# Kernel optimization log

Hardware: AMD Instinct MI355X
Metric: run time of the kernel (lower is better)

## Reference

```python
import jax, jax.numpy as jnp
import numpy as np

B, L, D = 4, 16384, 128          # batch, voxels per sample, d_model
DI, DS, DTR, K = 256, 16, 8, 4   # d_inner, d_state, dt_rank, conv kernel
N = B * L
EPS = 1e-5


def setup_inputs() -> dict:
    key = jax.random.key(0)
    ks = jax.random.split(key, 12)
    s = 0.02
    feats = jax.random.normal(ks[0], (N, D), jnp.float32)
    coords_xyz = jax.random.randint(ks[1], (N, 3), 0, 1024, jnp.int32)
    # per-batch Morton permutation + its inverse
    perm = jnp.stack([jax.random.permutation(jax.random.fold_in(ks[2], i), L) for i in range(B)]).astype(jnp.int32)
    inv_perm = jnp.argsort(perm, axis=1).astype(jnp.int32)
    return {
        'feats': feats,
        'pos_w': jax.random.normal(ks[3], (3, D), jnp.float32) * s,
        'pos_b': jnp.zeros((D,), jnp.float32),
        'rms_w': jnp.ones((D,), jnp.float32),
        'in_proj_w': jax.random.normal(ks[4], (D, 2 * DI), jnp.float32) * s,
        'conv_w': jax.random.normal(ks[5], (DI, K), jnp.float32) * s,
        'conv_b': jnp.zeros((DI,), jnp.float32),
        'x_proj_w': jax.random.normal(ks[6], (DI, DTR + 2 * DS), jnp.float32) * s,
        'dt_proj_w': jax.random.normal(ks[7], (DTR, DI), jnp.float32) * s,
        'dt_proj_b': jax.random.normal(ks[8], (DI,), jnp.float32) * 0.1,
        'A_log': jnp.log(jnp.broadcast_to(jnp.arange(1.0, DS + 1.0, dtype=jnp.float32), (DI, DS))),
        'D_param': jnp.ones((DI,), jnp.float32),
        'out_proj_w': jax.random.normal(ks[9], (DI, D), jnp.float32) * s,
        'ln_w': jnp.ones((D,), jnp.float32),
        'ln_b': jnp.zeros((D,), jnp.float32),
        'coords_xyz': coords_xyz,
        'perm': perm,
        'inv_perm': inv_perm,
    }


def _gssm(feats, pos_w, pos_b, rms_w, in_proj_w, conv_w, conv_b, x_proj_w,
          dt_proj_w, dt_proj_b, A_log, D_param, out_proj_w, ln_w, ln_b,
          coords_xyz, perm, inv_perm):
    # positional embedding of voxel coords
    pe = coords_xyz.astype(jnp.float32) @ pos_w + pos_b            # [N, D]
    h = (feats + pe).reshape(B, L, D)
    # gather into Morton order (per-batch fancy index)
    hm = jnp.take_along_axis(h, perm[:, :, None].astype(jnp.int32), axis=1)  # [B, L, D]
    # Mamba block: RMSNorm then mixer (block returns mixer output only)
    x = hm * jax.lax.rsqrt(jnp.mean(hm * hm, axis=-1, keepdims=True) + EPS) * rms_w
    xz = x @ in_proj_w                                             # [B, L, 2*DI]
    xi, z = xz[..., :DI], xz[..., DI:]
    # depthwise causal conv1d, kernel K
    xp = jnp.pad(xi, ((0, 0), (K - 1, 0), (0, 0)))
    xc = conv_b + sum(xp[:, j:j + L, :] * conv_w[:, j] for j in range(K))
    xc = jax.nn.silu(xc)                                           # [B, L, DI]
    dbc = xc @ x_proj_w                                            # [B, L, DTR+2*DS]
    dt, Bm, Cm = dbc[..., :DTR], dbc[..., DTR:DTR + DS], dbc[..., DTR + DS:]
    dt = jax.nn.softplus(dt @ dt_proj_w + dt_proj_b)               # [B, L, DI]
    A = -jnp.exp(A_log)                                            # [DI, DS]

    def step(hst, inp):
        x_t, dt_t, b_t, c_t = inp                                  # [B,DI],[B,DI],[B,DS],[B,DS]
        hst = jnp.exp(dt_t[..., None] * A) * hst + (dt_t * x_t)[..., None] * b_t[:, None, :]
        return hst, jnp.einsum('bds,bs->bd', hst, c_t)

    h0 = jnp.zeros((B, DI, DS), xc.dtype)
    _, ys = jax.lax.scan(step, h0, (xc.transpose(1, 0, 2), dt.transpose(1, 0, 2),
                                    Bm.transpose(1, 0, 2), Cm.transpose(1, 0, 2)))
    y = ys.transpose(1, 0, 2) + xc * D_param                       # [B, L, DI]
    y = y * jax.nn.silu(z)
    out = y @ out_proj_w                                           # [B, L, D]
    # scatter back to original voxel order
    out = jnp.take_along_axis(out, inv_perm[:, :, None].astype(jnp.int32), axis=1).reshape(N, D)
    # post-SSM LayerNorm
    mu = jnp.mean(out, axis=-1, keepdims=True)
    var = jnp.mean((out - mu) ** 2, axis=-1, keepdims=True)
    return (out - mu) * jax.lax.rsqrt(var + EPS) * ln_w + ln_b


def reference(feats, pos_w, pos_b, rms_w, in_proj_w, conv_w, conv_b, x_proj_w,
              dt_proj_w, dt_proj_b, A_log, D_param, out_proj_w, ln_w, ln_b,
              coords_xyz, perm, inv_perm):
    return _gssm(feats, pos_w, pos_b, rms_w, in_proj_w, conv_w, conv_b, x_proj_w,
                 dt_proj_w, dt_proj_b, A_log, D_param, out_proj_w, ln_w, ln_b,
                 coords_xyz, perm, inv_perm)
```

## Files before the change

kernel.cpp:

```cpp
#include <hip/hip_runtime.h>
#include <hip/hip_bf16.h>
#include <math.h>

#define B_   4
#define L_   16384
#define D_   128
#define DI_  256
#define DS_  16
#define DTR_ 8
#define N_   65536
#define NC_  128
#define LC_  128
#define TW_  16
#define TP_  260
#define EPS_ 1e-5f

typedef __hip_bfloat16 bf16;
typedef __attribute__((ext_vector_type(8))) short short8;
typedef __attribute__((ext_vector_type(4))) float f32x4;

__device__ __forceinline__ bool probe_bf16(const void* Dp) {
  return ((const unsigned*)Dp)[0] == 0x3F803F80u;
}
__device__ __forceinline__ float ldin(const void* p, size_t i, bool isb) {
  return isb ? __bfloat162float(((const bf16*)p)[i]) : ((const float*)p)[i];
}
__device__ __forceinline__ float4 ld4(const void* p, size_t i4, bool isb) {
  if (!isb) return ((const float4*)p)[i4];
  const ushort4 v = ((const ushort4*)p)[i4];
  float4 r;
  r.x = __uint_as_float((unsigned)v.x << 16);
  r.y = __uint_as_float((unsigned)v.y << 16);
  r.z = __uint_as_float((unsigned)v.z << 16);
  r.w = __uint_as_float((unsigned)v.w << 16);
  return r;
}
__device__ __forceinline__ void splitbf(float v, ushort& hi, ushort& lo) {
  bf16 h = __float2bfloat16(v);
  float rem = v - __bfloat162float(h);
  bf16 l = __float2bfloat16(rem);
  hi = *(ushort*)&h;
  lo = *(ushort*)&l;
}


__global__ __launch_bounds__(256) void k_xnorm(
    const void* __restrict__ feats, const void* __restrict__ pos_w,
    const void* __restrict__ pos_b, const void* __restrict__ rms_w,
    const int* __restrict__ coords, const int* __restrict__ perm,
    const void* __restrict__ Dprobe,
    ushort* __restrict__ xh, ushort* __restrict__ xl) {
  const bool isb = probe_bf16(Dprobe);
  int wv = threadIdx.x >> 6, lane = threadIdx.x & 63;
  int p = blockIdx.x * 4 + wv;
  int b = p >> 14;
  int srow = b * L_ + perm[p];
  float cx = (float)coords[srow*3+0];
  float cy = (float)coords[srow*3+1];
  float cz = (float)coords[srow*3+2];
  int i0 = lane, i1 = lane + 64;
  float h0 = ldin(feats,(size_t)srow*D_ + i0,isb) + cx*ldin(pos_w,i0,isb) + cy*ldin(pos_w,D_+i0,isb)
           + cz*ldin(pos_w,2*D_+i0,isb) + ldin(pos_b,i0,isb);
  float h1 = ldin(feats,(size_t)srow*D_ + i1,isb) + cx*ldin(pos_w,i1,isb) + cy*ldin(pos_w,D_+i1,isb)
           + cz*ldin(pos_w,2*D_+i1,isb) + ldin(pos_b,i1,isb);
  float ss = h0*h0 + h1*h1;
  #pragma unroll
  for (int off = 32; off; off >>= 1) ss += __shfl_xor(ss, off);
  float r = 1.0f / sqrtf(ss * (1.f/128.f) + EPS_);
  float v0 = h0 * r * ldin(rms_w,i0,isb);
  float v1 = h1 * r * ldin(rms_w,i1,isb);
  ushort a, bq;
  splitbf(v0, a, bq);
  xh[(size_t)p*D_ + i0] = a; xl[(size_t)p*D_ + i0] = bq;
  splitbf(v1, a, bq);
  xh[(size_t)p*D_ + i1] = a; xl[(size_t)p*D_ + i1] = bq;
}

__global__ __launch_bounds__(256) void k_prepw(
    const void* __restrict__ Win, const void* __restrict__ Dprobe,
    ushort* __restrict__ wth, ushort* __restrict__ wtl) {
  const bool isb = probe_bf16(Dprobe);
  int idx = blockIdx.x * 256 + threadIdx.x;
  int k = idx >> 9, n = idx & 511;
  float v = ldin(Win, (size_t)k*512 + n, isb);
  ushort a, b;
  splitbf(v, a, b);
  wth[(size_t)n*128 + k] = a;
  wtl[(size_t)n*128 + k] = b;
}

__global__ __launch_bounds__(256) void k_inproj(
    const ushort* __restrict__ xh, const ushort* __restrict__ xl,
    const ushort* __restrict__ wth, const ushort* __restrict__ wtl,
    float* __restrict__ xiT, float* __restrict__ zB) {
  __shared__ short Ah[64*136];
  __shared__ short Al[64*136];
  __shared__ short Bh[32*136];
  __shared__ short Bl[32*136];
  int tid = threadIdx.x;
  int T0 = blockIdx.x * 64;
  int lane = tid & 63, w = tid >> 6;
  {
    int k0 = (tid & 15) * 8;
    int m0 = tid >> 4;
    #pragma unroll
    for (int mi = 0; mi < 4; ++mi) {
      int m = m0 + 16*mi;
      *(short8*)&Ah[m*136 + k0] = *(const short8*)&xh[(size_t)(T0+m)*128 + k0];
      *(short8*)&Al[m*136 + k0] = *(const short8*)&xl[(size_t)(T0+m)*128 + k0];
    }
  }
  __syncthreads();
  int mloc = lane & 15, quad = lane >> 4;
  short8 afh[4], afl[4];
  #pragma unroll
  for (int ks = 0; ks < 4; ++ks) {
    int ka = ks*32 + quad*8;
    afh[ks] = *(const short8*)&Ah[(w*16 + mloc)*136 + ka];
    afl[ks] = *(const short8*)&Al[(w*16 + mloc)*136 + ka];
  }
  for (int ct = 0; ct < 16; ++ct) {
    int C0 = ct * 32;
    __syncthreads();
    {
      int k0 = (tid & 15) * 8;
      int n0 = tid >> 4;
      #pragma unroll
      for (int ni = 0; ni < 2; ++ni) {
        int n = n0 + 16*ni;
        *(short8*)&Bh[n*136 + k0] = *(const short8*)&wth[(size_t)(C0+n)*128 + k0];
        *(short8*)&Bl[n*136 + k0] = *(const short8*)&wtl[(size_t)(C0+n)*128 + k0];
      }
    }
    __syncthreads();
    #pragma unroll
    for (int nt = 0; nt < 2; ++nt) {
      f32x4 acc = {0.f, 0.f, 0.f, 0.f};
      #pragma unroll
      for (int ks = 0; ks < 4; ++ks) {
        int kb = ks*32 + quad*8;
        short8 bh = *(const short8*)&Bh[(nt*16 + mloc)*136 + kb];
        short8 bl = *(const short8*)&Bl[(nt*16 + mloc)*136 + kb];
        acc = __builtin_amdgcn_mfma_f32_16x16x32_bf16(afh[ks], bh, acc, 0, 0, 0);
        acc = __builtin_amdgcn_mfma_f32_16x16x32_bf16(afl[ks], bh, acc, 0, 0, 0);
        acc = __builtin_amdgcn_mfma_f32_16x16x32_bf16(afh[ks], bl, acc, 0, 0, 0);
      }
      int col = C0 + nt*16 + mloc;
      int trow = T0 + w*16 + quad*4;
      if (col < 256) {
        *(float4*)&xiT[(size_t)col*N_ + trow] = make_float4(acc[0], acc[1], acc[2], acc[3]);
      } else {
        int zc = col - 256;
        #pragma unroll
        for (int r = 0; r < 4; ++r)
          zB[(size_t)(trow + r)*256 + zc] = acc[r];
      }
    }
  }
}

__global__ __launch_bounds__(256) void k_conv_s(
    const float* __restrict__ xiT, const void* __restrict__ conv_w,
    const void* __restrict__ conv_b, const void* __restrict__ Dprobe,
    float* __restrict__ xcT) {
  const bool isb = probe_bf16(Dprobe);
  int idx = blockIdx.x * 256 + threadIdx.x;
  int c = idx >> 16;
  int t = idx & 65535;
  int l = t & (L_-1);
  const float* row = xiT + (size_t)c * N_;
  float acc = ldin(conv_b, c, isb);
  if (l >= 3) acc += row[t-3] * ldin(conv_w, c*4+0, isb);
  if (l >= 2) acc += row[t-2] * ldin(conv_w, c*4+1, isb);
  if (l >= 1) acc += row[t-1] * ldin(conv_w, c*4+2, isb);
  acc += row[t] * ldin(conv_w, c*4+3, isb);
  xcT[(size_t)c*N_ + t] = acc / (1.f + __expf(-acc));
}

__global__ __launch_bounds__(256) void k_xproj(
    const float* __restrict__ xcT, const void* __restrict__ xW,
    const void* __restrict__ dtW, const void* __restrict__ dtb,
    const void* __restrict__ Dprobe,
    float* __restrict__ dtT, float* __restrict__ BmB, float* __restrict__ CmB) {
  const bool isb = probe_bf16(Dprobe);
  __shared__ float lds[15488];
  int tid = threadIdx.x;
  int T0 = blockIdx.x * 128;
  int t = tid & 127, half = tid >> 7;
  #pragma unroll
  for (int p = 0; p < 10; ++p) {
    int idx = p*256 + tid;
    *(float4*)&lds[idx*4] = ld4(xW, idx, isb);
  }
  __syncthreads();
  float acc[40];
  #pragma unroll
  for (int q = 0; q < 40; ++q) acc[q] = 0.f;
  for (int c = 0; c < 128; c += 2) {
    int ch0 = half*128 + c, ch1 = ch0 + 1;
    float v0 = xcT[(size_t)ch0*N_ + T0 + t];
    float v1 = xcT[(size_t)ch1*N_ + T0 + t];
    const float* w0 = &lds[ch0*40];
    const float* w1 = &lds[ch1*40];
    #pragma unroll
    for (int q = 0; q < 10; ++q) {
      float4 a = *(const float4*)&w0[q*4];
      float4 b = *(const float4*)&w1[q*4];
      acc[q*4+0] += v0*a.x + v1*b.x;
      acc[q*4+1] += v0*a.y + v1*b.y;
      acc[q*4+2] += v0*a.z + v1*b.z;
      acc[q*4+3] += v0*a.w + v1*b.w;
    }
  }
  if (half == 1) {
    #pragma unroll
    for (int q = 0; q < 40; ++q) lds[10240 + t*41 + q] = acc[q];
  }
  __syncthreads();
  if (half == 0) {
    #pragma unroll
    for (int q = 0; q < 40; ++q) acc[q] += lds[10240 + t*41 + q];
  }
  __syncthreads();
  if (half == 0) {
    *(float4*)&BmB[(size_t)(T0+t)*16 + 0]  = make_float4(acc[8],  acc[9],  acc[10], acc[11]);
    *(float4*)&BmB[(size_t)(T0+t)*16 + 4]  = make_float4(acc[12], acc[13], acc[14], acc[15]);
    *(float4*)&BmB[(size_t)(T0+t)*16 + 8]  = make_float4(acc[16], acc[17], acc[18], acc[19]);
    *(float4*)&BmB[(size_t)(T0+t)*16 + 12] = make_float4(acc[20], acc[21], acc[22], acc[23]);
    *(float4*)&CmB[(size_t)(T0+t)*16 + 0]  = make_float4(acc[24], acc[25], acc[26], acc[27]);
    *(float4*)&CmB[(size_t)(T0+t)*16 + 4]  = make_float4(acc[28], acc[29], acc[30], acc[31]);
    *(float4*)&CmB[(size_t)(T0+t)*16 + 8]  = make_float4(acc[32], acc[33], acc[34], acc[35]);
    *(float4*)&CmB[(size_t)(T0+t)*16 + 12] = make_float4(acc[36], acc[37], acc[38], acc[39]);
    #pragma unroll
    for (int r = 0; r < 8; ++r) lds[10240 + t*9 + r] = acc[r];
  }
  #pragma unroll
  for (int p = 0; p < 8; ++p) lds[11392 + p*256 + tid] = ldin(dtW, p*256 + tid, isb);
  lds[13440 + tid] = ldin(dtb, tid, isb);
  __syncthreads();
  int t2 = tid & 127, dhalf = tid >> 7;
  float db[8];
  #pragma unroll
  for (int r = 0; r < 8; ++r) db[r] = lds[10240 + t2*9 + r];
  for (int dd = 0; dd < 128; ++dd) {
    int d = dhalf*128 + dd;
    float pre = lds[13440 + d];
    #pragma unroll
    for (int r = 0; r < 8; ++r) pre += db[r] * lds[11392 + r*256 + d];
    float sp = (pre > 20.f) ? pre : log1pf(__expf(pre));
    dtT[(size_t)d*N_ + T0 + t2] = sp;
  }
}

__global__ __launch_bounds__(256) void k_scan1(
    const float* __restrict__ dtT, const float* __restrict__ xcT,
    const float* __restrict__ BmB, const void* __restrict__ A_log,
    const void* __restrict__ Dprobe, float* __restrict__ Pb, float* __restrict__ Sb) {
  const bool isb = probe_bf16(Dprobe);
  __shared__ float sdt[TW_*TP_];
  __shared__ float sxc[TW_*TP_];
  __shared__ float sbm[LC_*16];
  int tid = threadIdx.x;
  int blk = blockIdx.x;
  int b = blk >> 7, ch = blk & 127;
  int T0 = b * L_ + ch * LC_;
  int d = tid;
  #pragma unroll
  for (int p = 0; p < 2; ++p) {
    int f = (p*256 + tid) * 4;
    *(float4*)&sbm[f] = *(const float4*)&BmB[(size_t)T0*16 + f];
  }
  float Al[16];
  #pragma unroll
  for (int s = 0; s < 16; ++s) Al[s] = -__expf(ldin(A_log, d*16 + s, isb));
  float h[16];
  #pragma unroll
  for (int s = 0; s < 16; ++s) h[s] = 0.f;
  float sumdt = 0.f;
  for (int it = 0; it < LC_; it += TW_) {
    __syncthreads();
    #pragma unroll
    for (int p = 0; p < 4; ++p) {
      int idx = p*256 + tid;
      int d2 = idx >> 2;
      int i4 = (idx & 3) * 4;
      float4 v = *(const float4*)&dtT[(size_t)d2*N_ + T0 + it + i4];
      float4 w = *(const float4*)&xcT[(size_t)d2*N_ + T0 + it + i4];
      sdt[(i4+0)*TP_ + d2] = v.x; sdt[(i4+1)*TP_ + d2] = v.y;
      sdt[(i4+2)*TP_ + d2] = v.z; sdt[(i4+3)*TP_ + d2] = v.w;
      sxc[(i4+0)*TP_ + d2] = w.x; sxc[(i4+1)*TP_ + d2] = w.y;
      sxc[(i4+2)*TP_ + d2] = w.z; sxc[(i4+3)*TP_ + d2] = w.w;
    }
    __syncthreads();
    #pragma unroll
    for (int i = 0; i < TW_; ++i) {
      float dtv = sdt[i*TP_ + d];
      float xcv = sxc[i*TP_ + d];
      sumdt += dtv;
      float du = dtv * xcv;
      const float* bmr = &sbm[(it+i)*16];
      #pragma unroll
      for (int s = 0; s < 16; ++s)
        h[s] = __expf(dtv * Al[s]) * h[s] + du * bmr[s];
    }
  }
  size_t rec = ((size_t)blk*256 + d) * 16;
  #pragma unroll
  for (int s = 0; s < 16; ++s) {
    Sb[rec + s] = h[s];
    Pb[rec + s] = __expf(Al[s] * sumdt);
  }
}

__global__ __launch_bounds__(256) void k_scan2(
    const float* __restrict__ Pb, const float* __restrict__ Sb, float* __restrict__ Hin) {
  int tid = blockIdx.x * 256 + threadIdx.x;
  int b = tid >> 12, r = tid & 4095;
  float h = 0.f;
  for (int ch = 0; ch < NC_; ++ch) {
    size_t rec = ((size_t)(b*NC_ + ch)) * 4096 + r;
    Hin[rec] = h;
    h = Pb[rec] * h + Sb[rec];
  }
}

__global__ __launch_bounds__(256) void k_scan3(
    const float* __restrict__ dtT, const float* __restrict__ xcT,
    const float* __restrict__ BmB, const float* __restrict__ CmB,
    const void* __restrict__ A_log, const void* __restrict__ Dp,
    const float* __restrict__ Hin, float* __restrict__ zyg) {
  const bool isb = probe_bf16(Dp);
  __shared__ float sdt[TW_*TP_];
  __shared__ float sxc[TW_*TP_];
  __shared__ float sbm[LC_*16];
  __shared__ float scm[LC_*16];
  int tid = threadIdx.x;
  int blk = blockIdx.x;
  int b = blk >> 7, ch = blk & 127;
  int T0 = b * L_ + ch * LC_;
  int d = tid;
  #pragma unroll
  for (int p = 0; p < 2; ++p) {
    int f = (p*256 + tid) * 4;
    *(float4*)&sbm[f] = *(const float4*)&BmB[(size_t)T0*16 + f];
    *(float4*)&scm[f] = *(const float4*)&CmB[(size_t)T0*16 + f];
  }
  float Al[16];
  #pragma unroll
  for (int s = 0; s < 16; ++s) Al[s] = -__expf(ldin(A_log, d*16 + s, isb));
  float h[16];
  size_t rec = ((size_t)blk*256 + d) * 16;
  #pragma unroll
  for (int s = 0; s < 16; ++s) h[s] = Hin[rec + s];
  float Dv = ldin(Dp, d, isb);
  for (int it = 0; it < LC_; it += TW_) {
    __syncthreads();
    #pragma unroll
    for (int p = 0; p < 4; ++p) {
      int idx = p*256 + tid;
      int d2 = idx >> 2;
      int i4 = (idx & 3) * 4;
      float4 v = *(const float4*)&dtT[(size_t)d2*N_ + T0 + it + i4];
      float4 w = *(const float4*)&xcT[(size_t)d2*N_ + T0 + it + i4];
      sdt[(i4+0)*TP_ + d2] = v.x; sdt[(i4+1)*TP_ + d2] = v.y;
      sdt[(i4+2)*TP_ + d2] = v.z; sdt[(i4+3)*TP_ + d2] = v.w;
      sxc[(i4+0)*TP_ + d2] = w.x; sxc[(i4+1)*TP_ + d2] = w.y;
      sxc[(i4+2)*TP_ + d2] = w.z; sxc[(i4+3)*TP_ + d2] = w.w;
    }
    __syncthreads();
    #pragma unroll
    for (int i = 0; i < TW_; ++i) {
      float dtv = sdt[i*TP_ + d];
      float xcv = sxc[i*TP_ + d];
      float du = dtv * xcv;
      const float* bmr = &sbm[(it+i)*16];
      const float* cmr = &scm[(it+i)*16];
      float y = 0.f;
      #pragma unroll
      for (int s = 0; s < 16; ++s) {
        h[s] = __expf(dtv * Al[s]) * h[s] + du * bmr[s];
        y += h[s] * cmr[s];
      }
      float yv = y + xcv * Dv;
      size_t zi = (size_t)(T0 + it + i)*256 + d;
      float zv = zyg[zi];
      float sil = zv / (1.f + __expf(-zv));
      zyg[zi] = yv * sil;
    }
  }
}

__global__ __launch_bounds__(256) void k_outproj(
    const float* __restrict__ yg, const void* __restrict__ W2,
    const void* __restrict__ Dprobe, float* __restrict__ outp) {
  const bool isb = probe_bf16(Dprobe);
  __shared__ float As[64*68];
  __shared__ float Bs[64*128];
  int tid = threadIdx.x;
  int T0 = blockIdx.x * 64;
  int tm = tid & 15, tn = tid >> 4;
  float acc[4][8] = {{0.f}};
  for (int kb = 0; kb < 256; kb += 64) {
    {
      int m = tid & 63, kq = tid >> 6;
      #pragma unroll
      for (int r = 0; r < 4; ++r) {
        int k0 = kq*16 + r*4;
        float4 v = *(const float4*)&yg[(size_t)(T0+m)*256 + kb + k0];
        As[(k0+0)*68+m] = v.x; As[(k0+1)*68+m] = v.y;
        As[(k0+2)*68+m] = v.z; As[(k0+3)*68+m] = v.w;
      }
      int n = (tid & 31)*4, kq2 = tid >> 5;
      #pragma unroll
      for (int p = 0; p < 8; ++p) {
        int k = kq2 + p*8;
        float4 w = ld4(W2, ((size_t)(kb+k)*128 + n) >> 2, isb);
        *(float4*)&Bs[k*128 + n] = w;
      }
    }
    __syncthreads();
    #pragma unroll 4
    for (int k = 0; k < 64; ++k) {
      float4 a  = *(const float4*)&As[k*68 + tm*4];
      float4 b0 = *(const float4*)&Bs[k*128 + tn*8];
      float4 b1 = *(const float4*)&Bs[k*128 + tn*8 + 4];
      float am[4] = {a.x, a.y, a.z, a.w};
      float bn[8] = {b0.x, b0.y, b0.z, b0.w, b1.x, b1.y, b1.z, b1.w};
      #pragma unroll
      for (int mi = 0; mi < 4; ++mi)
        #pragma unroll
        for (int ni = 0; ni < 8; ++ni)
          acc[mi][ni] += am[mi] * bn[ni];
    }
    __syncthreads();
  }
  #pragma unroll
  for (int mi = 0; mi < 4; ++mi) {
    size_t m = (size_t)(T0 + tm*4 + mi);
    *(float4*)&outp[m*128 + tn*8]     = make_float4(acc[mi][0], acc[mi][1], acc[mi][2], acc[mi][3]);
    *(float4*)&outp[m*128 + tn*8 + 4] = make_float4(acc[mi][4], acc[mi][5], acc[mi][6], acc[mi][7]);
  }
}

__global__ __launch_bounds__(256) void k_ln(
    const float* __restrict__ outp, const int* __restrict__ perm,
    const void* __restrict__ ln_w, const void* __restrict__ ln_b,
    const void* __restrict__ Dprobe, void* __restrict__ out) {
  const bool isb = probe_bf16(Dprobe);
  int wv = threadIdx.x >> 6, lane = threadIdx.x & 63;
  int p = blockIdx.x * 4 + wv;
  int b = p >> 14;
  int dest = b * L_ + perm[p];
  float v0 = outp[(size_t)p*128 + lane];
  float v1 = outp[(size_t)p*128 + lane + 64];
  float s1 = v0 + v1, s2 = v0*v0 + v1*v1;
  #pragma unroll
  for (int off = 32; off; off >>= 1) {
    s1 += __shfl_xor(s1, off);
    s2 += __shfl_xor(s2, off);
  }
  float mean = s1 * (1.f/128.f);
  float var  = s2 * (1.f/128.f) - mean*mean;
  float r = 1.0f / sqrtf(var + EPS_);
  float o0 = (v0 - mean)*r*ldin(ln_w,lane,isb)    + ldin(ln_b,lane,isb);
  float o1 = (v1 - mean)*r*ldin(ln_w,lane+64,isb) + ldin(ln_b,lane+64,isb);
  if (isb) {
    ((bf16*)out)[(size_t)dest*128 + lane]      = __float2bfloat16(o0);
    ((bf16*)out)[(size_t)dest*128 + lane + 64] = __float2bfloat16(o1);
  } else {
    ((float*)out)[(size_t)dest*128 + lane]      = o0;
    ((float*)out)[(size_t)dest*128 + lane + 64] = o1;
  }
}

extern "C" void kernel_launch(void* const* d_in, const int* in_sizes, int n_in,
                              void* d_out, int out_size, void* d_ws, size_t ws_size,
                              hipStream_t stream) {
  const void* feats    = d_in[0];
  const void* pos_w    = d_in[1];
  const void* pos_b    = d_in[2];
  const void* rms_w    = d_in[3];
  const void* in_proj  = d_in[4];
  const void* conv_w   = d_in[5];
  const void* conv_b   = d_in[6];
  const void* x_proj   = d_in[7];
  const void* dt_projw = d_in[8];
  const void* dt_projb = d_in[9];
  const void* A_log    = d_in[10];
  const void* D_param  = d_in[11];
  const void* out_proj = d_in[12];
  const void* ln_w     = d_in[13];
  const void* ln_b     = d_in[14];
  const int*  coords   = (const int*)d_in[15];
  const int*  perm     = (const int*)d_in[16];

  float* ws = (float*)d_ws;
  const size_t NN = (size_t)N_;
  ushort* xh  = (ushort*)ws;
  ushort* xl  = (ushort*)(ws + 64*NN);
  ushort* wth = (ushort*)(ws + 640*NN);
  ushort* wtl = (ushort*)(ws + 641*NN);
  float* Pb   = ws;
  float* Sb   = ws + 32*NN;
  float* Hin  = ws + 64*NN;
  float* BmB  = ws + 96*NN;
  float* CmB  = ws + 112*NN;
  float* xiT  = ws + 128*NN;
  float* dtT  = ws + 128*NN;
  float* outp = ws + 128*NN;
  float* zB   = ws + 384*NN;
  float* yg   = zB;
  float* xcT  = ws + 640*NN;

  k_prepw<<<256, 256, 0, stream>>>(in_proj, D_param, wth, wtl);
  k_xnorm<<<N_/4, 256, 0, stream>>>(feats, pos_w, pos_b, rms_w, coords, perm, D_param, xh, xl);
  k_inproj<<<N_/64, 256, 0, stream>>>(xh, xl, wth, wtl, xiT, zB);
  k_conv_s<<<(DI_*N_)/256, 256, 0, stream>>>(xiT, conv_w, conv_b, D_param, xcT);
  k_xproj<<<N_/128, 256, 0, stream>>>(xcT, x_proj, dt_projw, dt_projb, D_param, dtT, BmB, CmB);
  k_scan1<<<B_*NC_, 256, 0, stream>>>(dtT, xcT, BmB, A_log, D_param, Pb, Sb);
  k_scan2<<<64, 256, 0, stream>>>(Pb, Sb, Hin);
  k_scan3<<<B_*NC_, 256, 0, stream>>>(dtT, xcT, BmB, CmB, A_log, D_param, Hin, zB);
  k_outproj<<<N_/64, 256, 0, stream>>>(yg, out_proj, D_param, outp);
  k_ln<<<N_/4, 256, 0, stream>>>(outp, perm, ln_w, ln_b, D_param, d_out);
}
```

Before: 574.4 us.

## Move x_proj GEMM onto bf16 MFMA with split-precision hi/lo operands

The FMA-based x_proj projection is replaced by MFMA 16x16x32 bf16 instructions, using three-term hi/lo splitting to keep roughly fp32 accuracy. A small new kernel prepacks the x_proj weights into transposed bf16 hi/lo buffers padded to 48 columns. Tiles shrink from 128 to 64 tokens per block. The dt_proj weights are now read from global memory rather than staged in LDS. This aims to cut the cost of the scalar FMA loop, in exchange for an extra launch, conversion work and more global weight reads.

```diff
diff --git a/kernel.cpp b/kernel.cpp
--- a/kernel.cpp
+++ b/kernel.cpp
@@ -87,6 +87,19 @@
   splitbf(v, a, b);
   wth[(size_t)n*128 + k] = a;
   wtl[(size_t)n*128 + k] = b;
+}
+
+__global__ __launch_bounds__(256) void k_prepxw(
+    const void* __restrict__ xW, const void* __restrict__ Dprobe,
+    ushort* __restrict__ wxh, ushort* __restrict__ wxl) {
+  const bool isb = probe_bf16(Dprobe);
+  int idx = blockIdx.x * 256 + threadIdx.x;
+  int q = idx >> 8, c = idx & 255;
+  float v = (q < 40) ? ldin(xW, (size_t)c*40 + q, isb) : 0.f;
+  ushort a, b;
+  splitbf(v, a, b);
+  wxh[idx] = a;
+  wxl[idx] = b;
 }
 
 __global__ __launch_bounds__(256) void k_inproj(
@@ -178,77 +191,97 @@
 }
 
 __global__ __launch_bounds__(256) void k_xproj(
-    const float* __restrict__ xcT, const void* __restrict__ xW,
+    const float* __restrict__ xcT,
+    const ushort* __restrict__ wxh, const ushort* __restrict__ wxl,
     const void* __restrict__ dtW, const void* __restrict__ dtb,
     const void* __restrict__ Dprobe,
     float* __restrict__ dtT, float* __restrict__ BmB, float* __restrict__ CmB) {
   const bool isb = probe_bf16(Dprobe);
-  __shared__ float lds[15488];
-  int tid = threadIdx.x;
-  int T0 = blockIdx.x * 128;
-  int t = tid & 127, half = tid >> 7;
-  #pragma unroll
-  for (int p = 0; p < 10; ++p) {
-    int idx = p*256 + tid;
-    *(float4*)&lds[idx*4] = ld4(xW, idx, isb);
+  __shared__ ushort Ah[64*136];
+  __shared__ ushort Al[64*136];
+  __shared__ float s40[64*52];
+  const int tid = threadIdx.x;
+  const int lane = tid & 63, w = tid >> 6;
+  const int T0 = blockIdx.x * 64;
+  const int n15 = lane & 15, quad = lane >> 4;
+
+  short8 afh[8], afl[8];
+  #pragma unroll
+  for (int kh = 0; kh < 2; ++kh) {
+    if (kh) __syncthreads();
+    #pragma unroll
+    for (int p = 0; p < 4; ++p) {
+      int idx = p*256 + tid;
+      int cp = idx >> 4;
+      int t4 = idx & 15;
+      const float* base = &xcT[(size_t)(kh*128 + 2*cp)*N_ + T0 + t4*4];
+      float4 v0 = *(const float4*)base;
+      float4 v1 = *(const float4*)(base + N_);
+      uint* AH = (uint*)Ah;
+      uint* AL = (uint*)Al;
+      int r0 = t4*4;
+      ushort ha, la, hb, lb;
+      splitbf(v0.x, ha, la); splitbf(v1.x, hb, lb);
+      AH[(r0+0)*68 + cp] = (uint)ha | ((uint)hb << 16);
+      AL[(r0+0)*68 + cp] = (uint)la | ((uint)lb << 16);
+      splitbf(v0.y, ha, la); splitbf(v1.y, hb, lb);
+      AH[(r0+1)*68 + cp] = (uint)ha | ((uint)hb << 16);
+      AL[(r0+1)*68 + cp] = (uint)la | ((uint)lb << 16);
+      splitbf(v0.z, ha, la); splitbf(v1.z, hb, lb);
+      AH[(r0+2)*68 + cp] = (uint)ha | ((uint)hb << 16);
+      AL[(r0+2)*68 + cp] = (uint)la | ((uint)lb << 16);
+      splitbf(v0.w, ha, la); splitbf(v1.w, hb, lb);
+      AH[(r0+3)*68 + cp] = (uint)ha | ((uint)hb << 16);
+      AL[(r0+3)*68 + cp] = (uint)la | ((uint)lb << 16);
+    }
+    __syncthreads();
+    {
+      int mrow = w*16 + n15;
+      #pragma unroll
+      for (int ks = 0; ks < 4; ++ks) {
+        int ka = ks*32 + quad*8;
+        afh[kh*4+ks] = *(const short8*)&Ah[mrow*136 + ka];
+        afl[kh*4+ks] = *(const short8*)&Al[mrow*136 + ka];
+      }
+    }
+  }
+  #pragma unroll
+  for (int nt = 0; nt < 3; ++nt) {
+    f32x4 a = {0.f, 0.f, 0.f, 0.f};
+    size_t bb = (size_t)(nt*16 + n15)*256 + quad*8;
+    #pragma unroll
+    for (int ks = 0; ks < 8; ++ks) {
+      short8 bh = *(const short8*)&wxh[bb + ks*32];
+      short8 bl = *(const short8*)&wxl[bb + ks*32];
+      a = __builtin_amdgcn_mfma_f32_16x16x32_bf16(afh[ks], bh, a, 0, 0, 0);
+      a = __builtin_amdgcn_mfma_f32_16x16x32_bf16(afl[ks], bh, a, 0, 0, 0);
+      a = __builtin_amdgcn_mfma_f32_16x16x32_bf16(afh[ks], bl, a, 0, 0, 0);
+    }
+    #pragma unroll
+    for (int r = 0; r < 4; ++r)
+      s40[(w*16 + quad*4 + r)*52 + nt*16 + n15] = a[r];
   }
   __syncthreads();
-  float acc[40];
-  #pragma unroll
-  for (int q = 0; q < 40; ++q) acc[q] = 0.f;
-  for (int c = 0; c < 128; c += 2) {
-    int ch0 = half*128 + c, ch1 = ch0 + 1;
-    float v0 = xcT[(size_t)ch0*N_ + T0 + t];
-    float v1 = xcT[(size_t)ch1*N_ + T0 + t];
-    const float* w0 = &lds[ch0*40];
-    const float* w1 = &lds[ch1*40];
-    #pragma unroll
-    for (int q = 0; q < 10; ++q) {
-      float4 a = *(const float4*)&w0[q*4];
-      float4 b = *(const float4*)&w1[q*4];
-      acc[q*4+0] += v0*a.x + v1*b.x;
-      acc[q*4+1] += v0*a.y + v1*b.y;
-      acc[q*4+2] += v0*a.z + v1*b.z;
-      acc[q*4+3] += v0*a.w + v1*b.w;
-    }
-  }
-  if (half == 1) {
-    #pragma unroll
-    for (int q = 0; q < 40; ++q) lds[10240 + t*41 + q] = acc[q];
-  }
-  __syncthreads();
-  if (half == 0) {
-    #pragma unroll
-    for (int q = 0; q < 40; ++q) acc[q] += lds[10240 + t*41 + q];
-  }
-  __syncthreads();
-  if (half == 0) {
-    *(float4*)&BmB[(size_t)(T0+t)*16 + 0]  = make_float4(acc[8],  acc[9],  acc[10], acc[11]);
-    *(float4*)&BmB[(size_t)(T0+t)*16 + 4]  = make_float4(acc[12], acc[13], acc[14], acc[15]);
-    *(float4*)&BmB[(size_t)(T0+t)*16 + 8]  = make_float4(acc[16], acc[17], acc[18], acc[19]);
-    *(float4*)&BmB[(size_t)(T0+t)*16 + 12] = make_float4(acc[20], acc[21], acc[22], acc[23]);
-    *(float4*)&CmB[(size_t)(T0+t)*16 + 0]  = make_float4(acc[24], acc[25], acc[26], acc[27]);
-    *(float4*)&CmB[(size_t)(T0+t)*16 + 4]  = make_float4(acc[28], acc[29], acc[30], acc[31]);
-    *(float4*)&CmB[(size_t)(T0+t)*16 + 8]  = make_float4(acc[32], acc[33], acc[34], acc[35]);
-    *(float4*)&CmB[(size_t)(T0+t)*16 + 12] = make_float4(acc[36], acc[37], acc[38], acc[39]);
-    #pragma unroll
-    for (int r = 0; r < 8; ++r) lds[10240 + t*9 + r] = acc[r];
-  }
-  #pragma unroll
-  for (int p = 0; p < 8; ++p) lds[11392 + p*256 + tid] = ldin(dtW, p*256 + tid, isb);
-  lds[13440 + tid] = ldin(dtb, tid, isb);
-  __syncthreads();
-  int t2 = tid & 127, dhalf = tid >> 7;
-  float db[8];
-  #pragma unroll
-  for (int r = 0; r < 8; ++r) db[r] = lds[10240 + t2*9 + r];
-  for (int dd = 0; dd < 128; ++dd) {
-    int d = dhalf*128 + dd;
-    float pre = lds[13440 + d];
-    #pragma unroll
-    for (int r = 0; r < 8; ++r) pre += db[r] * lds[11392 + r*256 + d];
-    float sp = (pre > 20.f) ? pre : log1pf(__expf(pre));
-    dtT[(size_t)d*N_ + T0 + t2] = sp;
+  {
+    int t = tid >> 2, fq = tid & 3;
+    float4 bm = *(const float4*)&s40[t*52 + 8  + fq*4];
+    float4 cm = *(const float4*)&s40[t*52 + 24 + fq*4];
+    *(float4*)&BmB[(size_t)(T0+t)*16 + fq*4] = bm;
+    *(float4*)&CmB[(size_t)(T0+t)*16 + fq*4] = cm;
+  }
+  {
+    float4 d0 = *(const float4*)&s40[lane*52 + 0];
+    float4 d1 = *(const float4*)&s40[lane*52 + 4];
+    float dtv[8] = {d0.x, d0.y, d0.z, d0.w, d1.x, d1.y, d1.z, d1.w};
+    #pragma unroll 4
+    for (int dd = 0; dd < 64; ++dd) {
+      int d = w*64 + dd;
+      float pre = ldin(dtb, d, isb);
+      #pragma unroll
+      for (int r = 0; r < 8; ++r) pre += dtv[r] * ldin(dtW, r*256 + d, isb);
+      float sp = (pre > 20.f) ? pre : log1pf(__expf(pre));
+      dtT[(size_t)d*N_ + T0 + lane] = sp;
+    }
   }
 }
 
@@ -500,6 +533,8 @@
   ushort* xl  = (ushort*)(ws + 64*NN);
   ushort* wth = (ushort*)(ws + 640*NN);
   ushort* wtl = (ushort*)(ws + 641*NN);
+  ushort* wxh = (ushort*)ws;
+  ushort* wxl = ((ushort*)ws) + 48*256;
   float* Pb   = ws;
   float* Sb   = ws + 32*NN;
   float* Hin  = ws + 64*NN;
@@ -515,8 +550,9 @@
   k_prepw<<<256, 256, 0, stream>>>(in_proj, D_param, wth, wtl);
   k_xnorm<<<N_/4, 256, 0, stream>>>(feats, pos_w, pos_b, rms_w, coords, perm, D_param, xh, xl);
   k_inproj<<<N_/64, 256, 0, stream>>>(xh, xl, wth, wtl, xiT, zB);
+  k_prepxw<<<48, 256, 0, stream>>>(x_proj, D_param, wxh, wxl);
   k_conv_s<<<(DI_*N_)/256, 256, 0, stream>>>(xiT, conv_w, conv_b, D_param, xcT);
-  k_xproj<<<N_/128, 256, 0, stream>>>(xcT, x_proj, dt_projw, dt_projb, D_param, dtT, BmB, CmB);
+  k_xproj<<<N_/64, 256, 0, stream>>>(xcT, wxh, wxl, dt_projw, dt_projb, D_param, dtT, BmB, CmB);
   k_scan1<<<B_*NC_, 256, 0, stream>>>(dtT, xcT, BmB, A_log, D_param, Pb, Sb);
   k_scan2<<<64, 256, 0, stream>>>(Pb, Sb, Hin);
   k_scan3<<<B_*NC_, 256, 0, stream>>>(dtT, xcT, BmB, CmB, A_log, D_param, Hin, zB);
```

After: 571.5 us. No clear change (-0.5%).
